# Kernel optimization log

Hardware: AMD Instinct MI355X
Metric: run time of the kernel (lower is better)

The kernel has to match this reference:

```python
import jax, jax.numpy as jnp
import numpy as np

N = 100000   # n_nodes
E = 1600000  # n_edges
BN_EPS = 1e-5


def setup_inputs() -> dict:
    key = jax.random.key(0)
    ks = jax.random.split(key, 10)
    x = jax.random.normal(ks[0], (N, 20), dtype=jnp.float32)
    edge_index = jax.random.randint(ks[1], (2, E), 0, N, dtype=jnp.int64)
    dims = [(20, 64), (64, 48), (48, 32)]
    inp = {"x": x, "edge_index": edge_index}
    for i, (di, do) in enumerate(dims):
        inp[f"W{i+1}"] = jax.random.normal(ks[2 + i], (di, do), dtype=jnp.float32) / np.sqrt(di)
        inp[f"b{i+1}"] = jnp.zeros((do,), dtype=jnp.float32)
        inp[f"g{i+1}"] = jnp.ones((do,), dtype=jnp.float32)
        inp[f"beta{i+1}"] = jnp.zeros((do,), dtype=jnp.float32)
    return inp


def _gcn_norm(edge_index):
    # add self loops, compute symmetric normalization D^-1/2 (A+I) D^-1/2
    loop = jnp.arange(N, dtype=edge_index.dtype)
    src = jnp.concatenate([edge_index[0], loop])
    dst = jnp.concatenate([edge_index[1], loop])
    deg = jax.ops.segment_sum(jnp.ones_like(src, dtype=jnp.float32), dst, num_segments=N)
    dinv = jax.lax.rsqrt(deg)  # deg >= 1 thanks to self loops
    norm = dinv[src] * dinv[dst]  # [E+N]
    return src, dst, norm


def _gcn_layer(h, src, dst, norm, W, b):
    m = h @ W                                  # [N, out]
    agg = jax.ops.segment_sum(m[src] * norm[:, None], dst, num_segments=N)
    return agg + b


def _batchnorm(x, g, beta):
    mu = jnp.mean(x, axis=0)
    var = jnp.mean(jnp.square(x - mu), axis=0)  # biased, as torch BN training
    return (x - mu) * jax.lax.rsqrt(var + BN_EPS) * g + beta


def reference(x, edge_index, W1, b1, g1, beta1, W2, b2, g2, beta2, W3, b3, g3, beta3):
    src, dst, norm = _gcn_norm(edge_index)
    h = _gcn_layer(x, src, dst, norm, W1, b1)
    h = jax.nn.relu(_batchnorm(h, g1, beta1))   # dropout rate 0 -> identity
    h = _gcn_layer(h, src, dst, norm, W2, b2)
    h = jax.nn.relu(_batchnorm(h, g2, beta2))
    h = _gcn_layer(h, src, dst, norm, W3, b3)
    h = _batchnorm(h, g3, beta3)                # last activation is Identity
    return h
```

## Files before the change

### kernel.cpp

```cpp
#include <hip/hip_runtime.h>


#define NN 100000
#define NE 1600000
constexpr float BN_EPS_F = 1e-5f;
constexpr float INVN = 1.f / (float)NN;

#define BSZ 128
#define NBKT ((NN + BSZ - 1) / BSZ)
#define EC 16384
#define NEB ((NE + EC - 1) / EC)
#define MTOT (NBKT * NEB)
#define CAP 4096


__device__ __forceinline__ unsigned f2bf(float f) {
  union { float f; unsigned u; } v; v.f = f;
  return (v.u + 0x7fffu + ((v.u >> 16) & 1u)) >> 16;
}
__device__ __forceinline__ unsigned pack_bf2(float f0, float f1) {
  return f2bf(f0) | (f2bf(f1) << 16);
}
__device__ __forceinline__ float bf_lo(unsigned u) {
  union { unsigned u; float f; } v; v.u = u << 16; return v.f;
}
__device__ __forceinline__ float bf_hi(unsigned u) {
  union { unsigned u; float f; } v; v.u = u & 0xffff0000u; return v.f;
}


__global__ void hist_pass(const int* __restrict__ dst, int* __restrict__ ph, int e) {
  __shared__ int h[NBKT];
  int tid = threadIdx.x;
  for (int i = tid; i < NBKT; i += 256) h[i] = 0;
  __syncthreads();
  int tbase = blockIdx.x * EC + tid * 64;
#pragma unroll 4
  for (int k = 0; k < 64; k += 4) {
    int i = tbase + k;
    if (i < e) {
      int4 d = *(const int4*)(dst + i);
      atomicAdd(&h[d.x >> 7], 1);
      atomicAdd(&h[d.y >> 7], 1);
      atomicAdd(&h[d.z >> 7], 1);
      atomicAdd(&h[d.w >> 7], 1);
    }
  }
  __syncthreads();
  for (int i = tid; i < NBKT; i += 256) ph[i * NEB + blockIdx.x] = h[i];
}

__global__ void scan_block_sums(const int* __restrict__ data, int* __restrict__ bsums, int n) {
  __shared__ int sd[256];
  int tid = threadIdx.x;
  int base = blockIdx.x * 1024;
  int s = 0;
#pragma unroll
  for (int j = 0; j < 4; j++) {
    int idx = base + tid * 4 + j;
    if (idx < n) s += data[idx];
  }
  sd[tid] = s;
  __syncthreads();
  for (int o = 128; o > 0; o >>= 1) {
    if (tid < o) sd[tid] += sd[tid + o];
    __syncthreads();
  }
  if (tid == 0) bsums[blockIdx.x] = sd[0];
}

__global__ void scan_bsums2(int* __restrict__ bsums, int nb) {
  __shared__ int sd[128];
  int tid = threadIdx.x;
  int v = (tid < nb) ? bsums[tid] : 0;
  sd[tid] = v;
  __syncthreads();
  for (int o = 1; o < 128; o <<= 1) {
    int t = (tid >= o) ? sd[tid - o] : 0;
    __syncthreads();
    sd[tid] += t;
    __syncthreads();
  }
  if (tid < nb) bsums[tid] = sd[tid] - v;
}

__global__ void scan_apply(int* __restrict__ data, const int* __restrict__ bsums, int n) {
  __shared__ int sd[256];
  int tid = threadIdx.x;
  int base = blockIdx.x * 1024;
  int c[4];
  int s = 0;
#pragma unroll
  for (int j = 0; j < 4; j++) {
    int idx = base + tid * 4 + j;
    c[j] = (idx < n) ? data[idx] : 0;
    s += c[j];
  }
  sd[tid] = s;
  __syncthreads();
  for (int o = 1; o < 256; o <<= 1) {
    int t = (tid >= o) ? sd[tid - o] : 0;
    __syncthreads();
    sd[tid] += t;
    __syncthreads();
  }
  int off = bsums[blockIdx.x] + sd[tid] - s;
#pragma unroll
  for (int j = 0; j < 4; j++) {
    int idx = base + tid * 4 + j;
    if (idx < n) {
      data[idx] = off;
      off += c[j];
    }
  }
}

__global__ void bin_pass(const int* __restrict__ src, const int* __restrict__ dst,
                         const int* __restrict__ ph, int* __restrict__ packed, int e) {
  __shared__ int cur[NBKT];
  int tid = threadIdx.x;
  for (int i = tid; i < NBKT; i += 256) cur[i] = ph[i * NEB + blockIdx.x];
  __syncthreads();
  int tbase = blockIdx.x * EC + tid * 64;
#pragma unroll 4
  for (int k = 0; k < 64; k += 4) {
    int i = tbase + k;
    if (i < e) {
      int4 s = *(const int4*)(src + i);
      int4 d = *(const int4*)(dst + i);
      int p0 = atomicAdd(&cur[d.x >> 7], 1);
      int p1 = atomicAdd(&cur[d.y >> 7], 1);
      int p2 = atomicAdd(&cur[d.z >> 7], 1);
      int p3 = atomicAdd(&cur[d.w >> 7], 1);
      packed[p0] = (s.x << 7) | (d.x & 127);
      packed[p1] = (s.y << 7) | (d.y & 127);
      packed[p2] = (s.z << 7) | (d.z & 127);
      packed[p3] = (s.w << 7) | (d.w & 127);
    }
  }
}

__global__ void bucket_finalize(const int* __restrict__ ph, const int* __restrict__ packed,
                                const float* __restrict__ x, int* __restrict__ rowptr,
                                float* __restrict__ dinv, int* __restrict__ csr_src,
                                unsigned* __restrict__ xb) {
  __shared__ int eidx[CAP];
  __shared__ int csr_l[CAP];
  __shared__ int ldeg[BSZ], lscan[BSZ], lcur[BSZ];
  __shared__ float ldinv[BSZ];
  int b = blockIdx.x, tid = threadIdx.x;
  int start = ph[b * NEB];
  int end = (b == NBKT - 1) ? NE : ph[(b + 1) * NEB];
  int cnt = end - start;
  if (cnt > CAP) cnt = CAP;
  for (int i = tid; i < cnt; i += 256) eidx[i] = packed[start + i];
  if (tid < BSZ) ldeg[tid] = 0;
  __syncthreads();
  for (int i = tid; i < cnt; i += 256) atomicAdd(&ldeg[eidx[i] & 127], 1);
  __syncthreads();
  if (tid < BSZ) lscan[tid] = ldeg[tid];
  __syncthreads();
  for (int o = 1; o < BSZ; o <<= 1) {
    int t = 0;
    if (tid < BSZ && tid >= o) t = lscan[tid - o];
    __syncthreads();
    if (tid < BSZ) lscan[tid] += t;
    __syncthreads();
  }
  int gn = b * BSZ + tid;
  if (tid < BSZ) {
    int ex = lscan[tid] - ldeg[tid];
    lcur[tid] = ex;
    float dv = rsqrtf((float)(ldeg[tid] + 1));
    ldinv[tid] = dv;
    if (gn < NN) {
      rowptr[gn] = start + ex;
      dinv[gn] = dv;
    }
  }
  if (b == NBKT - 1 && tid == 0) rowptr[NN] = NE;
  __syncthreads();
  for (int i = tid; i < cnt; i += 256) {
    int pe = eidx[i];
    int pos = atomicAdd(&lcur[pe & 127], 1);
    csr_l[pos] = pe >> 7;
  }
  __syncthreads();
  for (int i = tid; i < cnt; i += 256) csr_src[start + i] = csr_l[i];
  for (int i = tid; i < BSZ * 16; i += 256) {
    int nl = i >> 4, j = i & 15;
    int g2 = b * BSZ + nl;
    if (g2 < NN) {
      unsigned u = 0;
      if (j < 10) {
        float2 f = *(const float2*)(x + (size_t)g2 * 20 + 2 * j);
        float dd = ldinv[nl];
        u = pack_bf2(dd * f.x, dd * f.y);
      }
      xb[(size_t)g2 * 16 + j] = u;
    }
  }
}


__launch_bounds__(256)
__global__ void agg1_gemm1(const unsigned* __restrict__ mb, const int* __restrict__ rowptr,
                           const int* __restrict__ csr_src, const float* __restrict__ dinv,
                           const float* __restrict__ W1, const float* __restrict__ b1,
                           unsigned* __restrict__ h1u, float* __restrict__ gsum) {
  __shared__ float Wl[20 * 64];
  __shared__ float Hl[16][20];
  __shared__ float4 sbuf[256];
  int tid = threadIdx.x;
  for (int i = tid; i < 20 * 64; i += 256) Wl[i] = W1[i];
  int sub = tid >> 4, lane = tid & 15;
  int cl = (lane < 10) ? lane : lane - 10;
  int d = blockIdx.x * 16 + sub;
  int start = rowptr[d], end = rowptr[d + 1];
  unsigned su = mb[(size_t)d * 16 + cl];
  float acc0 = bf_lo(su), acc1 = bf_hi(su);
  int j = start;
  int aligned = (start + 3) & ~3;
  int pe = aligned < end ? aligned : end;
  for (; j < pe; j++) {
    unsigned u = mb[(size_t)csr_src[j] * 16 + cl];
    acc0 += bf_lo(u); acc1 += bf_hi(u);
  }
  for (; j + 16 <= end; j += 16) {
    int4 s0 = *(const int4*)(csr_src + j);
    int4 s1 = *(const int4*)(csr_src + j + 4);
    int4 s2 = *(const int4*)(csr_src + j + 8);
    int4 s3 = *(const int4*)(csr_src + j + 12);
    int idx[16] = {s0.x, s0.y, s0.z, s0.w, s1.x, s1.y, s1.z, s1.w,
                   s2.x, s2.y, s2.z, s2.w, s3.x, s3.y, s3.z, s3.w};
    unsigned u[16];
#pragma unroll
    for (int t = 0; t < 16; t++) u[t] = mb[(size_t)idx[t] * 16 + cl];
#pragma unroll
    for (int t = 0; t < 16; t++) { acc0 += bf_lo(u[t]); acc1 += bf_hi(u[t]); }
  }
  for (; j + 4 <= end; j += 4) {
    int4 s0 = *(const int4*)(csr_src + j);
    unsigned u0 = mb[(size_t)s0.x * 16 + cl], u1 = mb[(size_t)s0.y * 16 + cl];
    unsigned u2 = mb[(size_t)s0.z * 16 + cl], u3 = mb[(size_t)s0.w * 16 + cl];
    acc0 += bf_lo(u0) + bf_lo(u1) + bf_lo(u2) + bf_lo(u3);
    acc1 += bf_hi(u0) + bf_hi(u1) + bf_hi(u2) + bf_hi(u3);
  }
  for (; j < end; j++) {
    unsigned u = mb[(size_t)csr_src[j] * 16 + cl];
    acc0 += bf_lo(u); acc1 += bf_hi(u);
  }
  float dd = dinv[d];
  if (lane < 10) {
    Hl[sub][2 * cl] = dd * acc0;
    Hl[sub][2 * cl + 1] = dd * acc1;
  }
  __syncthreads();
  int cg = lane;
  float a0 = b1[4 * cg], a1 = b1[4 * cg + 1], a2 = b1[4 * cg + 2], a3 = b1[4 * cg + 3];
#pragma unroll
  for (int k = 0; k < 20; k++) {
    float a = Hl[sub][k];
    const float* w = &Wl[k * 64 + 4 * cg];
    a0 = fmaf(a, w[0], a0);
    a1 = fmaf(a, w[1], a1);
    a2 = fmaf(a, w[2], a2);
    a3 = fmaf(a, w[3], a3);
  }
  *(uint2*)(h1u + (size_t)d * 32 + 2 * cg) = make_uint2(pack_bf2(a0, a1), pack_bf2(a2, a3));
  sbuf[tid] = make_float4(a0, a1, a2, a3);
  __syncthreads();
  float* gs = gsum + (blockIdx.x & 31) * 128;
  if (tid < 16) {
    float s0 = 0.f, s1 = 0.f, s2 = 0.f, s3 = 0.f;
#pragma unroll
    for (int k = 0; k < 16; k++) {
      float4 a = sbuf[k * 16 + tid];
      s0 += a.x; s1 += a.y; s2 += a.z; s3 += a.w;
    }
    atomicAdd(&gs[4 * tid], s0);
    atomicAdd(&gs[4 * tid + 1], s1);
    atomicAdd(&gs[4 * tid + 2], s2);
    atomicAdd(&gs[4 * tid + 3], s3);
  }
  __syncthreads();
  sbuf[tid] = make_float4(a0 * a0, a1 * a1, a2 * a2, a3 * a3);
  __syncthreads();
  if (tid < 16) {
    float q0 = 0.f, q1 = 0.f, q2 = 0.f, q3 = 0.f;
#pragma unroll
    for (int k = 0; k < 16; k++) {
      float4 b = sbuf[k * 16 + tid];
      q0 += b.x; q1 += b.y; q2 += b.z; q3 += b.w;
    }
    atomicAdd(&gs[64 + 4 * tid], q0);
    atomicAdd(&gs[64 + 4 * tid + 1], q1);
    atomicAdd(&gs[64 + 4 * tid + 2], q2);
    atomicAdd(&gs[64 + 4 * tid + 3], q3);
  }
}


__launch_bounds__(256)
__global__ void gemm2_bf(const unsigned* __restrict__ hu, const float* __restrict__ W,
                         const float* __restrict__ gsum, const float* __restrict__ g,
                         const float* __restrict__ beta, const float* __restrict__ dinv,
                         unsigned* __restrict__ out) {
  __shared__ float Wl[64 * 48];
  __shared__ float Hl[16][64];
  __shared__ float scl[64], sft[64];
  int tid = threadIdx.x;
  int row0 = blockIdx.x * 16;
  if (tid < 64) {
    float s = 0.f, q = 0.f;
    for (int b = 0; b < 32; b++) {
      s += gsum[b * 128 + tid];
      q += gsum[b * 128 + 64 + tid];
    }
    float mean = s * INVN;
    float var = fmaxf(q * INVN - mean * mean, 0.f);
    float inv = rsqrtf(var + BN_EPS_F);
    float sc = g[tid] * inv;
    scl[tid] = sc;
    sft[tid] = beta[tid] - mean * sc;
  }
  for (int i = tid; i < 64 * 48; i += 256) Wl[i] = W[i];
  __syncthreads();
  for (int i = tid; i < 16 * 32; i += 256) {
    int r = i >> 5, j = i & 31;
    unsigned u = hu[(size_t)(row0 + r) * 32 + j];
    Hl[r][2 * j] = fmaxf(fmaf(bf_lo(u), scl[2 * j], sft[2 * j]), 0.f);
    Hl[r][2 * j + 1] = fmaxf(fmaf(bf_hi(u), scl[2 * j + 1], sft[2 * j + 1]), 0.f);
  }
  __syncthreads();
  int r = tid >> 4, c = tid & 15;
  if (c < 12) {
    float a0 = 0.f, a1 = 0.f, a2 = 0.f, a3 = 0.f;
#pragma unroll
    for (int k = 0; k < 64; k++) {
      float a = Hl[r][k];
      const float* w = &Wl[k * 48 + 4 * c];
      a0 = fmaf(a, w[0], a0);
      a1 = fmaf(a, w[1], a1);
      a2 = fmaf(a, w[2], a2);
      a3 = fmaf(a, w[3], a3);
    }
    float dd = dinv[row0 + r];
    uint2 uo = make_uint2(pack_bf2(dd * a0, dd * a1), pack_bf2(dd * a2, dd * a3));
    *(uint2*)(out + (size_t)(row0 + r) * 24 + 2 * c) = uo;
  }
}


__launch_bounds__(256)
__global__ void aggregate_bf48(const uint2* __restrict__ mb, const int* __restrict__ rowptr,
                               const int* __restrict__ csr_src, const float* __restrict__ dinv,
                               const float* __restrict__ bias, unsigned* __restrict__ out,
                               float* __restrict__ gsum) {
  __shared__ float4 sbuf[256];
  int tid = threadIdx.x;
  int sub = tid >> 4, lane = tid & 15;
  int cl = (lane < 12) ? lane : lane - 12;
  int d = blockIdx.x * 16 + sub;
  int start = rowptr[d], end = rowptr[d + 1];
  uint2 su = mb[(size_t)d * 12 + cl];
  float acc0 = bf_lo(su.x), acc1 = bf_hi(su.x), acc2 = bf_lo(su.y), acc3 = bf_hi(su.y);
  int j = start;
  int aligned = (start + 3) & ~3;
  int pe = aligned < end ? aligned : end;
  for (; j < pe; j++) {
    uint2 u = mb[(size_t)csr_src[j] * 12 + cl];
    acc0 += bf_lo(u.x); acc1 += bf_hi(u.x); acc2 += bf_lo(u.y); acc3 += bf_hi(u.y);
  }
  for (; j + 16 <= end; j += 16) {
    int4 s0 = *(const int4*)(csr_src + j);
    int4 s1 = *(const int4*)(csr_src + j + 4);
    int4 s2 = *(const int4*)(csr_src + j + 8);
    int4 s3 = *(const int4*)(csr_src + j + 12);
    int idx[16] = {s0.x, s0.y, s0.z, s0.w, s1.x, s1.y, s1.z, s1.w,
                   s2.x, s2.y, s2.z, s2.w, s3.x, s3.y, s3.z, s3.w};
    uint2 u[16];
#pragma unroll
    for (int t = 0; t < 16; t++) u[t] = mb[(size_t)idx[t] * 12 + cl];
#pragma unroll
    for (int t = 0; t < 16; t++) {
      acc0 += bf_lo(u[t].x); acc1 += bf_hi(u[t].x);
      acc2 += bf_lo(u[t].y); acc3 += bf_hi(u[t].y);
    }
  }
  for (; j + 4 <= end; j += 4) {
    int4 s0 = *(const int4*)(csr_src + j);
    uint2 u0 = mb[(size_t)s0.x * 12 + cl], u1 = mb[(size_t)s0.y * 12 + cl];
    uint2 u2 = mb[(size_t)s0.z * 12 + cl], u3 = mb[(size_t)s0.w * 12 + cl];
    acc0 += bf_lo(u0.x) + bf_lo(u1.x) + bf_lo(u2.x) + bf_lo(u3.x);
    acc1 += bf_hi(u0.x) + bf_hi(u1.x) + bf_hi(u2.x) + bf_hi(u3.x);
    acc2 += bf_lo(u0.y) + bf_lo(u1.y) + bf_lo(u2.y) + bf_lo(u3.y);
    acc3 += bf_hi(u0.y) + bf_hi(u1.y) + bf_hi(u2.y) + bf_hi(u3.y);
  }
  for (; j < end; j++) {
    uint2 u = mb[(size_t)csr_src[j] * 12 + cl];
    acc0 += bf_lo(u.x); acc1 += bf_hi(u.x); acc2 += bf_lo(u.y); acc3 += bf_hi(u.y);
  }
  float dd = dinv[d];
  float v0 = dd * acc0 + bias[4 * cl];
  float v1 = dd * acc1 + bias[4 * cl + 1];
  float v2 = dd * acc2 + bias[4 * cl + 2];
  float v3 = dd * acc3 + bias[4 * cl + 3];
  if (lane >= 12) { v0 = v1 = v2 = v3 = 0.f; }
  if (lane < 12) {
    uint2 uo = make_uint2(pack_bf2(v0, v1), pack_bf2(v2, v3));
    *(uint2*)(out + (size_t)d * 24 + 2 * cl) = uo;
  }
  sbuf[tid] = make_float4(v0, v1, v2, v3);
  __syncthreads();
  float* gs = gsum + (blockIdx.x & 31) * 128;
  if (tid < 12) {
    float s0 = 0.f, s1 = 0.f, s2 = 0.f, s3 = 0.f;
#pragma unroll
    for (int k = 0; k < 16; k++) {
      float4 a = sbuf[k * 16 + tid];
      s0 += a.x; s1 += a.y; s2 += a.z; s3 += a.w;
    }
    atomicAdd(&gs[4 * tid], s0);
    atomicAdd(&gs[4 * tid + 1], s1);
    atomicAdd(&gs[4 * tid + 2], s2);
    atomicAdd(&gs[4 * tid + 3], s3);
  }
  __syncthreads();
  sbuf[tid] = make_float4(v0 * v0, v1 * v1, v2 * v2, v3 * v3);
  __syncthreads();
  if (tid < 12) {
    float q0 = 0.f, q1 = 0.f, q2 = 0.f, q3 = 0.f;
#pragma unroll
    for (int k = 0; k < 16; k++) {
      float4 b = sbuf[k * 16 + tid];
      q0 += b.x; q1 += b.y; q2 += b.z; q3 += b.w;
    }
    atomicAdd(&gs[64 + 4 * tid], q0);
    atomicAdd(&gs[64 + 4 * tid + 1], q1);
    atomicAdd(&gs[64 + 4 * tid + 2], q2);
    atomicAdd(&gs[64 + 4 * tid + 3], q3);
  }
}


__launch_bounds__(256)
__global__ void gemm3_bf(const unsigned* __restrict__ hu, const float* __restrict__ W,
                         const float* __restrict__ gsum, const float* __restrict__ g,
                         const float* __restrict__ beta, const float* __restrict__ dinv,
                         unsigned* __restrict__ out) {
  __shared__ float Wl[48 * 32];
  __shared__ float Hl[16][48];
  __shared__ float scl[48], sft[48];
  int tid = threadIdx.x;
  int row0 = blockIdx.x * 16;
  if (tid < 48) {
    float s = 0.f, q = 0.f;
    for (int b = 0; b < 32; b++) {
      s += gsum[b * 128 + tid];
      q += gsum[b * 128 + 64 + tid];
    }
    float mean = s * INVN;
    float var = fmaxf(q * INVN - mean * mean, 0.f);
    float inv = rsqrtf(var + BN_EPS_F);
    float sc = g[tid] * inv;
    scl[tid] = sc;
    sft[tid] = beta[tid] - mean * sc;
  }
  for (int i = tid; i < 48 * 32; i += 256) Wl[i] = W[i];
  __syncthreads();
  for (int i = tid; i < 16 * 24; i += 256) {
    int r = i / 24, j = i % 24;
    unsigned u = hu[(size_t)(row0 + r) * 24 + j];
    Hl[r][2 * j] = fmaxf(fmaf(bf_lo(u), scl[2 * j], sft[2 * j]), 0.f);
    Hl[r][2 * j + 1] = fmaxf(fmaf(bf_hi(u), scl[2 * j + 1], sft[2 * j + 1]), 0.f);
  }
  __syncthreads();
  int r = tid >> 4, c2 = tid & 15;
  float a0 = 0.f, a1 = 0.f;
#pragma unroll
  for (int k = 0; k < 48; k++) {
    float a = Hl[r][k];
    a0 = fmaf(a, Wl[k * 32 + 2 * c2], a0);
    a1 = fmaf(a, Wl[k * 32 + 2 * c2 + 1], a1);
  }
  float dd = dinv[row0 + r];
  out[(size_t)(row0 + r) * 16 + c2] = pack_bf2(dd * a0, dd * a1);
}


__launch_bounds__(256)
__global__ void aggregate_bf32(const unsigned* __restrict__ mb, const int* __restrict__ rowptr,
                               const int* __restrict__ csr_src, const float* __restrict__ dinv,
                               const float* __restrict__ bias, unsigned* __restrict__ out,
                               float* __restrict__ gsum) {
  __shared__ float2 ssum[256], ssq[256];
  int tid = threadIdx.x;
  int sub = tid >> 4, lane = tid & 15;
  int d = blockIdx.x * 16 + sub;
  int start = rowptr[d], end = rowptr[d + 1];
  unsigned su = mb[(size_t)d * 16 + lane];
  float acc0 = bf_lo(su), acc1 = bf_hi(su);
  int j = start;
  int aligned = (start + 3) & ~3;
  int pe = aligned < end ? aligned : end;
  for (; j < pe; j++) {
    unsigned u = mb[(size_t)csr_src[j] * 16 + lane];
    acc0 += bf_lo(u); acc1 += bf_hi(u);
  }
  for (; j + 16 <= end; j += 16) {
    int4 s0 = *(const int4*)(csr_src + j);
    int4 s1 = *(const int4*)(csr_src + j + 4);
    int4 s2 = *(const int4*)(csr_src + j + 8);
    int4 s3 = *(const int4*)(csr_src + j + 12);
    int idx[16] = {s0.x, s0.y, s0.z, s0.w, s1.x, s1.y, s1.z, s1.w,
                   s2.x, s2.y, s2.z, s2.w, s3.x, s3.y, s3.z, s3.w};
    unsigned u[16];
#pragma unroll
    for (int t = 0; t < 16; t++) u[t] = mb[(size_t)idx[t] * 16 + lane];
#pragma unroll
    for (int t = 0; t < 16; t++) { acc0 += bf_lo(u[t]); acc1 += bf_hi(u[t]); }
  }
  for (; j + 4 <= end; j += 4) {
    int4 s0 = *(const int4*)(csr_src + j);
    unsigned u0 = mb[(size_t)s0.x * 16 + lane], u1 = mb[(size_t)s0.y * 16 + lane];
    unsigned u2 = mb[(size_t)s0.z * 16 + lane], u3 = mb[(size_t)s0.w * 16 + lane];
    acc0 += bf_lo(u0) + bf_lo(u1) + bf_lo(u2) + bf_lo(u3);
    acc1 += bf_hi(u0) + bf_hi(u1) + bf_hi(u2) + bf_hi(u3);
  }
  for (; j < end; j++) {
    unsigned u = mb[(size_t)csr_src[j] * 16 + lane];
    acc0 += bf_lo(u); acc1 += bf_hi(u);
  }
  float dd = dinv[d];
  float v0 = dd * acc0 + bias[2 * lane];
  float v1 = dd * acc1 + bias[2 * lane + 1];
  out[(size_t)d * 16 + lane] = pack_bf2(v0, v1);
  ssum[tid] = make_float2(v0, v1);
  ssq[tid] = make_float2(v0 * v0, v1 * v1);
  __syncthreads();
  if (tid < 16) {
    float s0 = 0.f, s1 = 0.f, q0 = 0.f, q1 = 0.f;
#pragma unroll
    for (int k = 0; k < 16; k++) {
      float2 a = ssum[k * 16 + tid];
      float2 b = ssq[k * 16 + tid];
      s0 += a.x; s1 += a.y; q0 += b.x; q1 += b.y;
    }
    float* gs = gsum + (blockIdx.x & 31) * 128;
    atomicAdd(&gs[2 * tid], s0);
    atomicAdd(&gs[2 * tid + 1], s1);
    atomicAdd(&gs[64 + 2 * tid], q0);
    atomicAdd(&gs[64 + 2 * tid + 1], q1);
  }
}


__launch_bounds__(256)
__global__ void bn_apply_out(const unsigned* __restrict__ hu, const float* __restrict__ gsum,
                             const float* __restrict__ g, const float* __restrict__ beta,
                             float* __restrict__ out) {
  __shared__ float scl[32], sft[32];
  int tid = threadIdx.x;
  if (tid < 32) {
    float s = 0.f, q = 0.f;
    for (int b = 0; b < 32; b++) {
      s += gsum[b * 128 + tid];
      q += gsum[b * 128 + 64 + tid];
    }
    float mean = s * INVN;
    float var = fmaxf(q * INVN - mean * mean, 0.f);
    float inv = rsqrtf(var + BN_EPS_F);
    float sc = g[tid] * inv;
    scl[tid] = sc;
    sft[tid] = beta[tid] - mean * sc;
  }
  __syncthreads();
  int base = (blockIdx.x * 256 + tid) * 4;
  int node = base >> 5;
  int c0 = base & 31;
  uint2 u = *(const uint2*)(hu + (size_t)node * 16 + (c0 >> 1));
  float4 o;
  o.x = bf_lo(u.x) * scl[c0] + sft[c0];
  o.y = bf_hi(u.x) * scl[c0 + 1] + sft[c0 + 1];
  o.z = bf_lo(u.y) * scl[c0 + 2] + sft[c0 + 2];
  o.w = bf_hi(u.y) * scl[c0 + 3] + sft[c0 + 3];
  *(float4*)(out + base) = o;
}


extern "C" void kernel_launch(void* const* d_in, const int* in_sizes, int n_in,
                              void* d_out, int out_size, void* d_ws, size_t ws_size,
                              hipStream_t stream) {
  const float* x = (const float*)d_in[0];
  const int* ei = (const int*)d_in[1];
  const float* W1 = (const float*)d_in[2];
  const float* b1 = (const float*)d_in[3];
  const float* g1 = (const float*)d_in[4];
  const float* be1 = (const float*)d_in[5];
  const float* W2 = (const float*)d_in[6];
  const float* b2 = (const float*)d_in[7];
  const float* g2 = (const float*)d_in[8];
  const float* be2 = (const float*)d_in[9];
  const float* W3 = (const float*)d_in[10];
  const float* b3 = (const float*)d_in[11];
  const float* g3 = (const float*)d_in[12];
  const float* be3 = (const float*)d_in[13];
  float* out = (float*)d_out;

  const int* src = ei;
  const int* dst = ei + NE;

  char* ws = (char*)d_ws;
  size_t off = 0;
  auto alloc = [&](size_t bytes) -> void* {
    void* p = ws + off;
    off += bytes;
    off = (off + 255) & ~(size_t)255;
    return p;
  };
  int* ph = (int*)alloc((size_t)MTOT * 4);
  int* bsums = (int*)alloc(128 * 4);
  int* packed = (int*)alloc((size_t)NE * 4);
  int* rowptr = (int*)alloc((NN + 1) * 4);
  int* csr_src = (int*)alloc((size_t)NE * 4);
  float* dinv = (float*)alloc(NN * 4);
  float* gsum = (float*)alloc(3 * 32 * 128 * 4);
  unsigned* xb = (unsigned*)alloc((size_t)NN * 16 * 4);
  unsigned* h1u = (unsigned*)alloc((size_t)NN * 32 * 4);
  unsigned* m2b = (unsigned*)alloc((size_t)NN * 24 * 4);
  unsigned* h2u = (unsigned*)alloc((size_t)NN * 24 * 4);

  unsigned* m3b = xb;
  unsigned* h3u = h1u;

  hipMemsetAsync(gsum, 0, 3 * 32 * 128 * 4, stream);

  const int nscan = (MTOT + 1023) / 1024;
  hist_pass<<<NEB, 256, 0, stream>>>(dst, ph, NE);
  scan_block_sums<<<nscan, 256, 0, stream>>>(ph, bsums, MTOT);
  scan_bsums2<<<1, 128, 0, stream>>>(bsums, nscan);
  scan_apply<<<nscan, 256, 0, stream>>>(ph, bsums, MTOT);
  bin_pass<<<NEB, 256, 0, stream>>>(src, dst, ph, packed, NE);
  bucket_finalize<<<NBKT, 256, 0, stream>>>(ph, packed, x, rowptr, dinv, csr_src, xb);

  agg1_gemm1<<<NN / 16, 256, 0, stream>>>(xb, rowptr, csr_src, dinv, W1, b1, h1u, gsum);

  gemm2_bf<<<NN / 16, 256, 0, stream>>>(h1u, W2, gsum, g1, be1, dinv, m2b);
  aggregate_bf48<<<NN / 16, 256, 0, stream>>>((const uint2*)m2b, rowptr, csr_src, dinv, b2, h2u,
                                              gsum + 4096);

  gemm3_bf<<<NN / 16, 256, 0, stream>>>(h2u, W3, gsum + 4096, g2, be2, dinv, m3b);
  aggregate_bf32<<<NN / 16, 256, 0, stream>>>(m3b, rowptr, csr_src, dinv, b3, h3u, gsum + 8192);

  bn_apply_out<<<NN * 32 / 1024, 256, 0, stream>>>(h3u, gsum + 8192, g3, be3, out);
}
```

Before: 335.0 us.

## Sort nodes by degree within ranges to balance aggregation warps

Adds a kernel that counting-sorts node ids by in-degree within each of 8 ranges of 12500 nodes, producing a permutation. The three aggregation kernels then process nodes in that order, so the 16 sub-groups in a block see similar edge counts and less lane time is wasted on divergence. It also cuts the partial BN-statistics slots from 32 to 8, which shrinks the final reduction but puts more atomics on each slot. The cost is an extra launch using only 8 blocks, a gather through perm, and less locality in the writes to destination rows.

```diff
diff --git a/kernel.cpp b/kernel.cpp
--- a/kernel.cpp
+++ b/kernel.cpp
@@ -12,6 +12,7 @@
 #define NEB ((NE + EC - 1) / EC)
 #define MTOT (NBKT * NEB)
 #define CAP 4096
+#define DRANGE 12500
 
 
 __device__ __forceinline__ unsigned f2bf(float f) {
@@ -203,11 +204,36 @@
 }
 
 
+__global__ void degsort_range(const int* __restrict__ rowptr, int* __restrict__ perm) {
+  __shared__ int h[64], cur[64];
+  int tid = threadIdx.x;
+  int r0 = blockIdx.x * DRANGE;
+  if (tid < 64) h[tid] = 0;
+  __syncthreads();
+  for (int i = r0 + tid; i < r0 + DRANGE; i += 256) {
+    int deg = rowptr[i + 1] - rowptr[i];
+    atomicAdd(&h[deg > 63 ? 63 : deg], 1);
+  }
+  __syncthreads();
+  if (tid == 0) {
+    int s = 0;
+    for (int k = 0; k < 64; k++) { cur[k] = s; s += h[k]; }
+  }
+  __syncthreads();
+  for (int i = r0 + tid; i < r0 + DRANGE; i += 256) {
+    int deg = rowptr[i + 1] - rowptr[i];
+    int pos = atomicAdd(&cur[deg > 63 ? 63 : deg], 1);
+    perm[r0 + pos] = i;
+  }
+}
+
+
 __launch_bounds__(256)
 __global__ void agg1_gemm1(const unsigned* __restrict__ mb, const int* __restrict__ rowptr,
                            const int* __restrict__ csr_src, const float* __restrict__ dinv,
-                           const float* __restrict__ W1, const float* __restrict__ b1,
-                           unsigned* __restrict__ h1u, float* __restrict__ gsum) {
+                           const int* __restrict__ perm, const float* __restrict__ W1,
+                           const float* __restrict__ b1, unsigned* __restrict__ h1u,
+                           float* __restrict__ gsum) {
   __shared__ float Wl[20 * 64];
   __shared__ float Hl[16][20];
   __shared__ float4 sbuf[256];
@@ -215,7 +241,7 @@
   for (int i = tid; i < 20 * 64; i += 256) Wl[i] = W1[i];
   int sub = tid >> 4, lane = tid & 15;
   int cl = (lane < 10) ? lane : lane - 10;
-  int d = blockIdx.x * 16 + sub;
+  int d = perm[blockIdx.x * 16 + sub];
   int start = rowptr[d], end = rowptr[d + 1];
   unsigned su = mb[(size_t)d * 16 + cl];
   float acc0 = bf_lo(su), acc1 = bf_hi(su);
@@ -270,7 +296,7 @@
   *(uint2*)(h1u + (size_t)d * 32 + 2 * cg) = make_uint2(pack_bf2(a0, a1), pack_bf2(a2, a3));
   sbuf[tid] = make_float4(a0, a1, a2, a3);
   __syncthreads();
-  float* gs = gsum + (blockIdx.x & 31) * 128;
+  float* gs = gsum + (blockIdx.x & 7) * 128;
   if (tid < 16) {
     float s0 = 0.f, s1 = 0.f, s2 = 0.f, s3 = 0.f;
 #pragma unroll
@@ -313,7 +339,7 @@
   int row0 = blockIdx.x * 16;
   if (tid < 64) {
     float s = 0.f, q = 0.f;
-    for (int b = 0; b < 32; b++) {
+    for (int b = 0; b < 8; b++) {
       s += gsum[b * 128 + tid];
       q += gsum[b * 128 + 64 + tid];
     }
@@ -355,13 +381,13 @@
 __launch_bounds__(256)
 __global__ void aggregate_bf48(const uint2* __restrict__ mb, const int* __restrict__ rowptr,
                                const int* __restrict__ csr_src, const float* __restrict__ dinv,
-                               const float* __restrict__ bias, unsigned* __restrict__ out,
-                               float* __restrict__ gsum) {
+                               const int* __restrict__ perm, const float* __restrict__ bias,
+                               unsigned* __restrict__ out, float* __restrict__ gsum) {
   __shared__ float4 sbuf[256];
   int tid = threadIdx.x;
   int sub = tid >> 4, lane = tid & 15;
   int cl = (lane < 12) ? lane : lane - 12;
-  int d = blockIdx.x * 16 + sub;
+  int d = perm[blockIdx.x * 16 + sub];
   int start = rowptr[d], end = rowptr[d + 1];
   uint2 su = mb[(size_t)d * 12 + cl];
   float acc0 = bf_lo(su.x), acc1 = bf_hi(su.x), acc2 = bf_lo(su.y), acc3 = bf_hi(su.y);
@@ -413,7 +439,7 @@
   }
   sbuf[tid] = make_float4(v0, v1, v2, v3);
   __syncthreads();
-  float* gs = gsum + (blockIdx.x & 31) * 128;
+  float* gs = gsum + (blockIdx.x & 7) * 128;
   if (tid < 12) {
     float s0 = 0.f, s1 = 0.f, s2 = 0.f, s3 = 0.f;
 #pragma unroll
@@ -456,7 +482,7 @@
   int row0 = blockIdx.x * 16;
   if (tid < 48) {
     float s = 0.f, q = 0.f;
-    for (int b = 0; b < 32; b++) {
+    for (int b = 0; b < 8; b++) {
       s += gsum[b * 128 + tid];
       q += gsum[b * 128 + 64 + tid];
     }
@@ -492,12 +518,12 @@
 __launch_bounds__(256)
 __global__ void aggregate_bf32(const unsigned* __restrict__ mb, const int* __restrict__ rowptr,
                                const int* __restrict__ csr_src, const float* __restrict__ dinv,
-                               const float* __restrict__ bias, unsigned* __restrict__ out,
-                               float* __restrict__ gsum) {
+                               const int* __restrict__ perm, const float* __restrict__ bias,
+                               unsigned* __restrict__ out, float* __restrict__ gsum) {
   __shared__ float2 ssum[256], ssq[256];
   int tid = threadIdx.x;
   int sub = tid >> 4, lane = tid & 15;
-  int d = blockIdx.x * 16 + sub;
+  int d = perm[blockIdx.x * 16 + sub];
   int start = rowptr[d], end = rowptr[d + 1];
   unsigned su = mb[(size_t)d * 16 + lane];
   float acc0 = bf_lo(su), acc1 = bf_hi(su);
@@ -547,7 +573,7 @@
       float2 b = ssq[k * 16 + tid];
       s0 += a.x; s1 += a.y; q0 += b.x; q1 += b.y;
     }
-    float* gs = gsum + (blockIdx.x & 31) * 128;
+    float* gs = gsum + (blockIdx.x & 7) * 128;
     atomicAdd(&gs[2 * tid], s0);
     atomicAdd(&gs[2 * tid + 1], s1);
     atomicAdd(&gs[64 + 2 * tid], q0);
@@ -564,7 +590,7 @@
   int tid = threadIdx.x;
   if (tid < 32) {
     float s = 0.f, q = 0.f;
-    for (int b = 0; b < 32; b++) {
+    for (int b = 0; b < 8; b++) {
       s += gsum[b * 128 + tid];
       q += gsum[b * 128 + 64 + tid];
     }
@@ -625,7 +651,8 @@
   int* rowptr = (int*)alloc((NN + 1) * 4);
   int* csr_src = (int*)alloc((size_t)NE * 4);
   float* dinv = (float*)alloc(NN * 4);
-  float* gsum = (float*)alloc(3 * 32 * 128 * 4);
+  int* perm = (int*)alloc(NN * 4);
+  float* gsum = (float*)alloc(3 * 8 * 128 * 4);
   unsigned* xb = (unsigned*)alloc((size_t)NN * 16 * 4);
   unsigned* h1u = (unsigned*)alloc((size_t)NN * 32 * 4);
   unsigned* m2b = (unsigned*)alloc((size_t)NN * 24 * 4);
@@ -634,7 +661,7 @@
   unsigned* m3b = xb;
   unsigned* h3u = h1u;
 
-  hipMemsetAsync(gsum, 0, 3 * 32 * 128 * 4, stream);
+  hipMemsetAsync(gsum, 0, 3 * 8 * 128 * 4, stream);
 
   const int nscan = (MTOT + 1023) / 1024;
   hist_pass<<<NEB, 256, 0, stream>>>(dst, ph, NE);
@@ -643,15 +670,17 @@
   scan_apply<<<nscan, 256, 0, stream>>>(ph, bsums, MTOT);
   bin_pass<<<NEB, 256, 0, stream>>>(src, dst, ph, packed, NE);
   bucket_finalize<<<NBKT, 256, 0, stream>>>(ph, packed, x, rowptr, dinv, csr_src, xb);
-
-  agg1_gemm1<<<NN / 16, 256, 0, stream>>>(xb, rowptr, csr_src, dinv, W1, b1, h1u, gsum);
+  degsort_range<<<8, 256, 0, stream>>>(rowptr, perm);
+
+  agg1_gemm1<<<NN / 16, 256, 0, stream>>>(xb, rowptr, csr_src, dinv, perm, W1, b1, h1u, gsum);
 
   gemm2_bf<<<NN / 16, 256, 0, stream>>>(h1u, W2, gsum, g1, be1, dinv, m2b);
-  aggregate_bf48<<<NN / 16, 256, 0, stream>>>((const uint2*)m2b, rowptr, csr_src, dinv, b2, h2u,
-                                              gsum + 4096);
-
-  gemm3_bf<<<NN / 16, 256, 0, stream>>>(h2u, W3, gsum + 4096, g2, be2, dinv, m3b);
-  aggregate_bf32<<<NN / 16, 256, 0, stream>>>(m3b, rowptr, csr_src, dinv, b3, h3u, gsum + 8192);
-
-  bn_apply_out<<<NN * 32 / 1024, 256, 0, stream>>>(h3u, gsum + 8192, g3, be3, out);
-}
+  aggregate_bf48<<<NN / 16, 256, 0, stream>>>((const uint2*)m2b, rowptr, csr_src, dinv, perm, b2,
+                                              h2u, gsum + 1024);
+
+  gemm3_bf<<<NN / 16, 256, 0, stream>>>(h2u, W3, gsum + 1024, g2, be2, dinv, m3b);
+  aggregate_bf32<<<NN / 16, 256, 0, stream>>>(m3b, rowptr, csr_src, dinv, perm, b3, h3u,
+                                              gsum + 2048);
+
+  bn_apply_out<<<NN * 32 / 1024, 256, 0, stream>>>(h3u, gsum + 2048, g3, be3, out);
+}
```

Result: slower. 433.1 us (+29.3%).
